# Kernel tuning notes

Hardware: AMD Instinct MI355X
Metric: run time of the kernel (lower is better)

Reference implementation:

```python
import jax, jax.numpy as jnp
import numpy as np

B, N, DIM = 32, 1024, 512
HEADS, HEAD_DIM = 8, 64
MLP_HIDDEN = 2048
MAX_DIST = 7
TABLE_SIZE = (2 * MAX_DIST + 1) ** 2  # 225


def setup_inputs() -> dict:
    key = jax.random.key(0)
    ks = jax.random.split(key, 8)
    return {
        "x": jax.random.normal(ks[0], (B, N, DIM), jnp.float32),
        "qkv_w": jax.random.normal(ks[1], (3 * DIM, DIM), jnp.float32) * 0.02,
        "proj_w": jax.random.normal(ks[2], (DIM, DIM), jnp.float32) * 0.02,
        "proj_b": jnp.zeros((DIM,), jnp.float32),
        "mlp_w1": jax.random.normal(ks[3], (MLP_HIDDEN, DIM), jnp.float32) * 0.02,
        "mlp_b1": jnp.zeros((MLP_HIDDEN,), jnp.float32),
        "mlp_w2": jax.random.normal(ks[4], (DIM, MLP_HIDDEN), jnp.float32) * 0.02,
        "mlp_b2": jnp.zeros((DIM,), jnp.float32),
        "norm1_g": jnp.ones((DIM,), jnp.float32),
        "norm1_b": jnp.zeros((DIM,), jnp.float32),
        "norm2_g": jnp.ones((DIM,), jnp.float32),
        "norm2_b": jnp.zeros((DIM,), jnp.float32),
        "bias_table": jax.random.normal(ks[5], (TABLE_SIZE, HEADS), jnp.float32) * 0.02,
        "height": 32,
        "width": 32,
    }


def _rel_pos_index(height, width):
    # exact replication of RelativePositionBias index math (numpy, trace-time)
    coords = np.stack(np.meshgrid(np.arange(height), np.arange(width), indexing="ij"))  # [2,H,W]
    flat = coords.reshape(2, -1)                         # [2,N]
    rel = flat[:, :, None] - flat[:, None, :]            # [2,N,N]
    rel = rel.transpose(1, 2, 0).copy()                  # [N,N,2]
    rel[:, :, 0] += height - 1
    rel[:, :, 1] += width - 1
    rel[:, :, 0] *= 2 * width - 1
    idx = np.clip(rel.sum(-1), 0, TABLE_SIZE - 1)
    return jnp.asarray(idx, jnp.int32)                   # [N,N]


def _layernorm(x, g, b, eps=1e-5):
    mu = x.mean(-1, keepdims=True)
    var = ((x - mu) ** 2).mean(-1, keepdims=True)
    return (x - mu) * jax.lax.rsqrt(var + eps) * g + b


def reference(x, qkv_w, proj_w, proj_b, mlp_w1, mlp_b1, mlp_w2, mlp_b2,
              norm1_g, norm1_b, norm2_g, norm2_b, bias_table, height, width):
    scale = HEAD_DIM ** -0.5
    idx = _rel_pos_index(height, width)
    bias = bias_table[idx]                               # [N,N,heads]
    bias = jnp.transpose(bias, (2, 0, 1))                # [heads,N,N]

    shortcut = x
    h = _layernorm(x, norm1_g, norm1_b)
    qkv = h @ qkv_w.T                                    # [B,N,3*DIM]
    qkv = qkv.reshape(x.shape[0], x.shape[1], 3, HEADS, HEAD_DIM)
    qkv = jnp.transpose(qkv, (2, 0, 3, 1, 4))            # [3,B,h,N,d]
    q, k, v = qkv[0], qkv[1], qkv[2]
    attn = jnp.einsum("bhnd,bhmd->bhnm", q, k) * scale
    attn = attn + bias[None]
    attn = jax.nn.softmax(attn, axis=-1)
    o = jnp.einsum("bhnm,bhmd->bhnd", attn, v)           # [B,h,N,d]
    o = jnp.transpose(o, (0, 2, 1, 3)).reshape(x.shape)  # [B,N,DIM]
    o = o @ proj_w.T + proj_b
    x = shortcut + o

    shortcut = x
    h = _layernorm(x, norm2_g, norm2_b)
    h = jax.nn.gelu(h @ mlp_w1.T + mlp_b1, approximate=False)
    h = h @ mlp_w2.T + mlp_b2
    return shortcut + h
```

## Files before the change

kernel.cpp:

```cpp
#include <hip/hip_runtime.h>

typedef short bf16x8 __attribute__((ext_vector_type(8)));
typedef float f32x4 __attribute__((ext_vector_type(4)));
typedef unsigned short us8 __attribute__((ext_vector_type(8)));
typedef unsigned short us2 __attribute__((ext_vector_type(2)));

__device__ __forceinline__ float bf2f(unsigned short u) {
    union { unsigned i; float f; } v; v.i = ((unsigned)u) << 16; return v.f;
}
__device__ __forceinline__ unsigned short f2bf(float f) {
    union { float f; unsigned i; } v; v.f = f;
    unsigned r = v.i + 0x7fffu + ((v.i >> 16) & 1u);
    return (unsigned short)(r >> 16);
}
__device__ __forceinline__ float ldflex(const void* p, int isf32, long i) {
    return isf32 ? ((const float*)p)[i] : bf2f(((const unsigned short*)p)[i]);
}
__device__ __forceinline__ float gelu_exact(float v) {
    return 0.5f * v * (1.0f + erff(v * 0.70710678118654752f));
}
__device__ __forceinline__ us8 pack8u(const float* s) {
    us8 r;
    #pragma unroll
    for (int i = 0; i < 8; ++i) r[i] = f2bf(s[i]);
    return r;
}

__device__ __forceinline__ void gld16(const void* g, void* l) {
    typedef __attribute__((address_space(1))) void GV;
    typedef __attribute__((address_space(3))) void LV;
    __builtin_amdgcn_global_load_lds((GV*)g, (LV*)l, 16, 0, 0);
}

struct SniffArgs { const void* p[13]; int n[13]; };

__global__ __launch_bounds__(64) void sniff_all(SniffArgs a, int* __restrict__ flags)
{
    const unsigned short* buf = (const unsigned short*)a.p[blockIdx.x];
    const int n_elems = a.n[blockIdx.x];
    __shared__ int cnt[3];
    if (threadIdx.x < 3) cnt[threadIdx.x] = 0;
    __syncthreads();
    int K = n_elems / 2; if (K > 1024) K = 1024; if (K < 1) K = 1;
    int ins = 0, ne = 0, no = 0;
    for (int i = threadIdx.x; i < K; i += 64) {
        const unsigned lo = buf[2 * i], hi = buf[2 * i + 1];
        const unsigned e = (lo >> 7) & 0xFF;
        ins += (lo != 0 && (e < 90 || e > 160)) ? 1 : 0;
        ne  += (lo != 0);
        no  += (hi != 0);
    }
    atomicAdd(&cnt[0], ins); atomicAdd(&cnt[1], ne); atomicAdd(&cnt[2], no);
    __syncthreads();
    if (threadIdx.x == 0)
        flags[blockIdx.x] = (cnt[0] * 10 > K) || (cnt[1] * 10 < K && cnt[2] * 2 > K);
}

struct CvtArgs { const void* src[7]; void* dst[7]; int fidx[7]; int n[7]; int tobf[7]; };

__global__ __launch_bounds__(256) void convert_params(CvtArgs a, const int* __restrict__ flags)
{
    const int t = blockIdx.y;
    const int i0 = (blockIdx.x * 256 + threadIdx.x) * 8;
    if (i0 >= a.n[t]) return;
    const int f = flags[a.fidx[t]];
    float v[8];
    if (f) {
        const float* s = (const float*)a.src[t] + i0;
        *(f32x4*)&v[0] = *(const f32x4*)s;
        *(f32x4*)&v[4] = *(const f32x4*)(s + 4);
    } else {
        us8 u = *(const us8*)((const unsigned short*)a.src[t] + i0);
        #pragma unroll
        for (int i = 0; i < 8; ++i) v[i] = bf2f(u[i]);
    }
    if (a.tobf[t]) {
        *(us8*)((unsigned short*)a.dst[t] + i0) = pack8u(v);
    } else {
        float* d = (float*)a.dst[t] + i0;
        *(f32x4*)d       = *(f32x4*)&v[0];
        *(f32x4*)(d + 4) = *(f32x4*)&v[4];
    }
}

__global__ __launch_bounds__(256) void gemm_bf16(
    const unsigned short* __restrict__ A, const unsigned short* __restrict__ W,
    void* __restrict__ C, int Nout, int K,
    const float* __restrict__ bias,
    const void* resid, const int* rflag, long resid_row0,
    int act, int out_bf16)
{
    __shared__ unsigned short As[128 * 32];
    __shared__ unsigned short Bs[128 * 32];
    const int tid  = threadIdx.x;
    const int lane = tid & 63, wv = tid >> 6;
    const int wrow = wv >> 1, wcol = wv & 1;
    const int fm = lane & 15, quad = lane >> 4;

    const int gx = gridDim.x;
    const int nwg = gx * gridDim.y;
    int lin = blockIdx.y * gx + blockIdx.x;
    lin = (lin & 7) * (nwg >> 3) + (lin >> 3);
    const int bm = (lin / gx) * 128, bn = (lin % gx) * 128;

    const int sr = tid >> 2;
    const int sb = (tid & 3) * 16;
    const char* Ab = (const char*)A;
    const char* Wb = (const char*)W;
    char* AsB = (char*)As;
    char* BsB = (char*)Bs;
    const long a0 = ((long)(bm + sr) * K) * 2 + sb;
    const long a1 = ((long)(bm + 64 + sr) * K) * 2 + sb;
    const long b0 = ((long)(bn + sr) * K) * 2 + sb;
    const long b1 = ((long)(bn + 64 + sr) * K) * 2 + sb;
    const int ld = tid * 16;

    f32x4 acc[4][4] = {};

    const int Kb = K * 2;
    for (int k0b = 0; k0b < Kb; k0b += 64) {
        __syncthreads();
        gld16(Ab + a0 + k0b, AsB + ld);
        gld16(Ab + a1 + k0b, AsB + 4096 + ld);
        gld16(Wb + b0 + k0b, BsB + ld);
        gld16(Wb + b1 + k0b, BsB + 4096 + ld);
        __syncthreads();

        bf16x8 af[4], bw[4];
        #pragma unroll
        for (int t = 0; t < 4; ++t) {
            af[t] = *(const bf16x8*)&As[(wrow * 64 + t * 16 + fm) * 32 + quad * 8];
            bw[t] = *(const bf16x8*)&Bs[(wcol * 64 + t * 16 + fm) * 32 + quad * 8];
        }
        #pragma unroll
        for (int i = 0; i < 4; ++i)
            #pragma unroll
            for (int j = 0; j < 4; ++j)
                acc[i][j] = __builtin_amdgcn_mfma_f32_16x16x32_bf16(
                                af[i], bw[j], acc[i][j], 0, 0, 0);
    }

    const int crow0 = bm + wrow * 64, ccol0 = bn + wcol * 64;
    if (out_bf16) {
        unsigned short* Cb = (unsigned short*)C;
        #pragma unroll
        for (int j = 0; j < 4; ++j) {
            const int col = ccol0 + j * 16 + fm;
            const float bv = bias ? bias[col] : 0.0f;
            #pragma unroll
            for (int i = 0; i < 4; ++i)
                #pragma unroll
                for (int r = 0; r < 4; ++r) {
                    const int row = crow0 + i * 16 + quad * 4 + r;
                    float v = acc[i][j][r] + bv;
                    if (act) v = gelu_exact(v);
                    Cb[(long)row * Nout + col] = f2bf(v);
                }
        }
    } else {
        float* Cf = (float*)C;
        const int rfl = resid ? (rflag ? *rflag : 1) : 1;
        #pragma unroll
        for (int j = 0; j < 4; ++j) {
            const int col = ccol0 + j * 16 + fm;
            const float bv = bias ? bias[col] : 0.0f;
            #pragma unroll
            for (int i = 0; i < 4; ++i)
                #pragma unroll
                for (int r = 0; r < 4; ++r) {
                    const int row = crow0 + i * 16 + quad * 4 + r;
                    float v = acc[i][j][r] + bv;
                    if (act)   v = gelu_exact(v);
                    if (resid) v += ldflex(resid, rfl, (resid_row0 + row) * (long)Nout + col);
                    Cf[(long)row * Nout + col] = v;
                }
        }
    }
}

__global__ __launch_bounds__(256) void layernorm_512(
    const void* __restrict__ x, const int* __restrict__ xflag, long row0,
    const void* __restrict__ g, const int* __restrict__ gflag,
    const void* __restrict__ b, const int* __restrict__ bflag,
    unsigned short* __restrict__ o)
{
    const int row = blockIdx.x;
    const int tid = threadIdx.x;
    const int xf = xflag ? *xflag : 1;
    const long base = (row0 + row) * 512 + tid * 2;
    const float vx = ldflex(x, xf, base);
    const float vy = ldflex(x, xf, base + 1);
    float s  = vx + vy;
    float s2 = vx * vx + vy * vy;
    #pragma unroll
    for (int off = 32; off > 0; off >>= 1) {
        s  += __shfl_down(s, off);
        s2 += __shfl_down(s2, off);
    }
    __shared__ float ss[4], ss2[4];
    if ((tid & 63) == 0) { ss[tid >> 6] = s; ss2[tid >> 6] = s2; }
    __syncthreads();
    const float ts   = ss[0] + ss[1] + ss[2] + ss[3];
    const float ts2  = ss2[0] + ss2[1] + ss2[2] + ss2[3];
    const float mean = ts * (1.0f / 512.0f);
    const float var  = ts2 * (1.0f / 512.0f) - mean * mean;
    const float rstd = rsqrtf(var + 1e-5f);
    const int gf = *gflag, bff = *bflag;
    us2 r;
    r[0] = f2bf((vx - mean) * rstd * ldflex(g, gf, tid * 2)     + ldflex(b, bff, tid * 2));
    r[1] = f2bf((vy - mean) * rstd * ldflex(g, gf, tid * 2 + 1) + ldflex(b, bff, tid * 2 + 1));
    *(us2*)(o + (long)row * 512 + tid * 2) = r;
}

__global__ __launch_bounds__(256, 5) void attn_mfma(
    const unsigned short* __restrict__ qkv,
    const void* __restrict__ table, const int* __restrict__ tflag,
    unsigned short* __restrict__ o)
{
    __shared__ unsigned short Ks[512 * 8];
    __shared__ unsigned short Vt[64 * 72];
    __shared__ unsigned short Pl[4][16 * 72];
    __shared__ float Tbh[225];

    const int tid  = threadIdx.x;
    const int lane = tid & 63, wv = tid >> 6;
    const int fm = lane & 15, quad = lane >> 4;

    const int hw    = blockIdx.x + gridDim.x * (blockIdx.y + gridDim.y * blockIdx.z);
    const int total = gridDim.x * gridDim.y * gridDim.z;
    const int lin   = (hw & 7) * (total >> 3) + (hw >> 3);
    const int q0 = (lin & 15) * 64;
    const int h  = (lin >> 4) & 7;
    const int b  = lin >> 7;

    {
        const int tf = *tflag;
        if (tid < 225) Tbh[tid] = ldflex(table, tf, tid * 8 + h);
    }

    bf16x8 qa[2];
    {
        const unsigned short* qb = &qkv[(long)((b * 1024 + q0 + wv * 16 + fm) * 3) * 512
                                        + h * 64 + quad * 8];
        qa[0] = *(const bf16x8*)qb;
        qa[1] = *(const bf16x8*)(qb + 32);
    }

    int base_r[4];
    #pragma unroll
    for (int r = 0; r < 4; ++r) {
        const int qi = q0 + wv * 16 + quad * 4 + r;
        base_r[r] = 63 * (qi >> 5) + (qi & 31) + 1984;
    }

    const int kc_fm   = tid & 15;
    const int kc_quad = (tid >> 4) & 3;
    const int kc_ch   = (tid >> 6) & 1;
    const int kc_c0   = (tid >> 7) & 1;
    const char* qkvB  = (const char*)qkv;
    long ksrc = (((long)(b * 1024 + kc_c0 * 16 + kc_fm) * 3 + 1) * 512
                 + h * 64 + kc_ch * 32 + kc_quad * 8) * 2;

    const int key_v = tid & 63;
    const int dv    = (tid >> 6) * 16;
    long vsrc = (((long)(b * 1024 + key_v) * 3 + 2) * 512 + h * 64 + dv) * 2;

    char* KsB = (char*)Ks;

    f32x4 acc[4] = {};
    float mrow[4] = {-1e30f, -1e30f, -1e30f, -1e30f};
    float lrow[4] = {};

    for (int kt = 0; kt < 16; ++kt) {
        const int k0 = kt * 64;
        __syncthreads();
        us8 v0 = *(const us8*)(qkvB + vsrc);
        us8 v1 = *(const us8*)(qkvB + vsrc + 16);
        gld16(qkvB + ksrc,         KsB + tid * 16);
        gld16(qkvB + ksrc + 98304, KsB + 4096 + tid * 16);
        ksrc += 196608; vsrc += 196608;
        #pragma unroll
        for (int i = 0; i < 8; ++i) Vt[(dv + i) * 72 + key_v] = v0[i];
        #pragma unroll
        for (int i = 0; i < 8; ++i) Vt[(dv + 8 + i) * 72 + key_v] = v1[i];
        __syncthreads();

        f32x4 sv[4];
        __builtin_amdgcn_s_setprio(1);
        #pragma unroll
        for (int c = 0; c < 4; ++c) {
            f32x4 z = {};
            z = __builtin_amdgcn_mfma_f32_16x16x32_bf16(
                    qa[0], *(const bf16x8*)&Ks[(((c * 2 + 0) * 4 + quad) * 16 + fm) * 8],
                    z, 0, 0, 0);
            z = __builtin_amdgcn_mfma_f32_16x16x32_bf16(
                    qa[1], *(const bf16x8*)&Ks[(((c * 2 + 1) * 4 + quad) * 16 + fm) * 8],
                    z, 0, 0, 0);
            sv[c] = z;
        }
        __builtin_amdgcn_s_setprio(0);

        #pragma unroll
        for (int c = 0; c < 4; ++c) {
            const int kj = k0 + c * 16 + fm;
            const int sub = 63 * (kj >> 5) + (kj & 31);
            #pragma unroll
            for (int r = 0; r < 4; ++r) {
                int idx = base_r[r] - sub;
                idx = idx > 224 ? 224 : idx;
                sv[c][r] = fmaf(sv[c][r], 0.125f, Tbh[idx]);
            }
        }

        float alpha[4];
        #pragma unroll
        for (int r = 0; r < 4; ++r) {
            float mr = fmaxf(fmaxf(sv[0][r], sv[1][r]), fmaxf(sv[2][r], sv[3][r]));
            #pragma unroll
            for (int off = 1; off < 16; off <<= 1) mr = fmaxf(mr, __shfl_xor(mr, off));
            const float mnew = fmaxf(mrow[r], mr);
            alpha[r] = __expf(mrow[r] - mnew);
            mrow[r] = mnew;
            float ps = 0.0f;
            #pragma unroll
            for (int c = 0; c < 4; ++c) {
                const float p = __expf(sv[c][r] - mnew);
                sv[c][r] = p;
                ps += p;
            }
            #pragma unroll
            for (int off = 1; off < 16; off <<= 1) ps += __shfl_xor(ps, off);
            lrow[r] = lrow[r] * alpha[r] + ps;
        }

        unsigned short* Pw = Pl[wv];
        #pragma unroll
        for (int c = 0; c < 4; ++c)
            #pragma unroll
            for (int r = 0; r < 4; ++r)
                Pw[(quad * 4 + r) * 72 + c * 16 + fm] = f2bf(sv[c][r]);

        const bf16x8 ap0 = *(const bf16x8*)&Pw[fm * 72 + quad * 8];
        const bf16x8 ap1 = *(const bf16x8*)&Pw[fm * 72 + 32 + quad * 8];
        __builtin_amdgcn_s_setprio(1);
        #pragma unroll
        for (int c = 0; c < 4; ++c) {
            #pragma unroll
            for (int r = 0; r < 4; ++r) acc[c][r] *= alpha[r];
            acc[c] = __builtin_amdgcn_mfma_f32_16x16x32_bf16(
                        ap0, *(const bf16x8*)&Vt[(c * 16 + fm) * 72 + quad * 8], acc[c], 0, 0, 0);
            acc[c] = __builtin_amdgcn_mfma_f32_16x16x32_bf16(
                        ap1, *(const bf16x8*)&Vt[(c * 16 + fm) * 72 + 32 + quad * 8], acc[c], 0, 0, 0);
        }
        __builtin_amdgcn_s_setprio(0);
    }

    float rinv[4];
    #pragma unroll
    for (int r = 0; r < 4; ++r) rinv[r] = 1.0f / lrow[r];
    #pragma unroll
    for (int c = 0; c < 4; ++c)
        #pragma unroll
        for (int r = 0; r < 4; ++r)
            o[(long)(b * 1024 + q0 + wv * 16 + quad * 4 + r) * 512 + h * 64 + c * 16 + fm]
                = f2bf(acc[c][r] * rinv[r]);
}

extern "C" void kernel_launch(void* const* d_in, const int* in_sizes, int n_in,
                              void* d_out, int out_size, void* d_ws, size_t ws_size,
                              hipStream_t stream)
{
    (void)n_in; (void)out_size;
    float* out = (float*)d_out;

    constexpr int B = 32, N = 1024;

    int* flags = (int*)d_ws;
    {
        SniffArgs sa;
        for (int t = 0; t < 13; ++t) { sa.p[t] = d_in[t]; sa.n[t] = in_sizes[t]; }
        sniff_all<<<13, 64, 0, stream>>>(sa, flags);
    }

    unsigned short* Wq = (unsigned short*)((char*)d_ws + 256);
    unsigned short* Wp = Wq + 786432;
    unsigned short* W1 = Wp + 262144;
    unsigned short* W2 = W1 + 1048576;
    float* Bp = (float*)(W2 + 1048576);
    float* B1 = Bp + 512;
    float* B2 = B1 + 2048;
    char* scr = (char*)(B2 + 512);
    scr = (char*)(((size_t)scr + 255) & ~(size_t)255);

    {
        CvtArgs ca;
        ca.src[0] = d_in[1]; ca.dst[0] = Wq; ca.fidx[0] = 1; ca.n[0] = 786432;  ca.tobf[0] = 1;
        ca.src[1] = d_in[2]; ca.dst[1] = Wp; ca.fidx[1] = 2; ca.n[1] = 262144;  ca.tobf[1] = 1;
        ca.src[2] = d_in[4]; ca.dst[2] = W1; ca.fidx[2] = 4; ca.n[2] = 1048576; ca.tobf[2] = 1;
        ca.src[3] = d_in[6]; ca.dst[3] = W2; ca.fidx[3] = 6; ca.n[3] = 1048576; ca.tobf[3] = 1;
        ca.src[4] = d_in[3]; ca.dst[4] = Bp; ca.fidx[4] = 3; ca.n[4] = 512;     ca.tobf[4] = 0;
        ca.src[5] = d_in[5]; ca.dst[5] = B1; ca.fidx[5] = 5; ca.n[5] = 2048;    ca.tobf[5] = 0;
        ca.src[6] = d_in[7]; ca.dst[6] = B2; ca.fidx[6] = 7; ca.n[6] = 512;     ca.tobf[6] = 0;
        convert_params<<<dim3(512, 7), 256, 0, stream>>>(ca, flags);
    }

    const size_t fixed = (size_t)(scr - (char*)d_ws);
    const size_t per_batch = (size_t)N * 3072 * 2;
    int bpc = (int)((ws_size - fixed) / per_batch);
    if (bpc < 1) bpc = 1;
    if (bpc > B) bpc = B;

    unsigned short* Ln = (unsigned short*)scr;
    unsigned short* Hd = Ln + (size_t)bpc * N * 512;
    unsigned short* Ao = Hd + (size_t)bpc * N * 2048;

    for (int b0 = 0; b0 < B; b0 += bpc) {
        const int nb   = (B - b0) < bpc ? (B - b0) : bpc;
        const int rows = nb * N;
        const long r0  = (long)b0 * N;

        layernorm_512<<<rows, 256, 0, stream>>>(
            d_in[0], flags + 0, r0, d_in[8], flags + 8, d_in[9], flags + 9, Ln);
        gemm_bf16<<<dim3(12, rows / 128), 256, 0, stream>>>(
            Ln, Wq, Hd, 1536, 512, nullptr, nullptr, nullptr, 0, 0, 1);
        attn_mfma<<<dim3(16, 8, nb), 256, 0, stream>>>(
            Hd, d_in[12], flags + 12, Ao);
        gemm_bf16<<<dim3(4, rows / 128), 256, 0, stream>>>(
            Ao, Wp, out + r0 * 512, 512, 512,
            Bp, d_in[0], flags + 0, r0, 0, 0);
    }

    for (int b0 = 0; b0 < B; b0 += bpc) {
        const int nb   = (B - b0) < bpc ? (B - b0) : bpc;
        const int rows = nb * N;
        const long r0  = (long)b0 * N;

        layernorm_512<<<rows, 256, 0, stream>>>(
            out + r0 * 512, nullptr, 0, d_in[10], flags + 10, d_in[11], flags + 11, Ln);
        gemm_bf16<<<dim3(16, rows / 128), 256, 0, stream>>>(
            Ln, W1, Hd, 2048, 512, B1, nullptr, nullptr, 0, 1, 1);
        gemm_bf16<<<dim3(4, rows / 128), 256, 0, stream>>>(
            Hd, W2, out + r0 * 512, 512, 2048,
            B2, out + r0 * 512, nullptr, 0, 0, 0);
    }
}
```

Before: 938.9 us.

## Double-buffer GEMM LDS tiles and restructure attention loads, bias, rowsum and packing

The GEMM now double-buffers its A/W LDS tiles, issuing the next k-slice load before the MFMAs and keeping one barrier per iteration. The attention kernel register-prefetches the next K/V tile, reads the relative-position bias from incrementally updated indices with contiguous table reads, and computes the softmax row sum with an MFMA against a ones vector instead of shuffle reductions. It also converts to bf16 with v_cvt_pk_bf16_f32 for the P tile and the output. The costs are more LDS (lower GEMM occupancy), more registers for prefetch, and the bf16-rounded P being used in the row sum.

```diff
diff --git a/kernel.cpp b/kernel.cpp
--- a/kernel.cpp
+++ b/kernel.cpp
@@ -24,6 +24,11 @@
     #pragma unroll
     for (int i = 0; i < 8; ++i) r[i] = f2bf(s[i]);
     return r;
+}
+__device__ __forceinline__ unsigned cvtpk_bf16(float lo, float hi) {
+    unsigned u;
+    asm("v_cvt_pk_bf16_f32 %0, %1, %2" : "=v"(u) : "v"(lo), "v"(hi));
+    return u;
 }
 
 __device__ __forceinline__ void gld16(const void* g, void* l) {
@@ -90,8 +95,8 @@
     const void* resid, const int* rflag, long resid_row0,
     int act, int out_bf16)
 {
-    __shared__ unsigned short As[128 * 32];
-    __shared__ unsigned short Bs[128 * 32];
+    __shared__ unsigned short As[2][128 * 32];
+    __shared__ unsigned short Bs[2][128 * 32];
     const int tid  = threadIdx.x;
     const int lane = tid & 63, wv = tid >> 6;
     const int wrow = wv >> 1, wcol = wv & 1;
@@ -107,30 +112,37 @@
     const int sb = (tid & 3) * 16;
     const char* Ab = (const char*)A;
     const char* Wb = (const char*)W;
-    char* AsB = (char*)As;
-    char* BsB = (char*)Bs;
     const long a0 = ((long)(bm + sr) * K) * 2 + sb;
     const long a1 = ((long)(bm + 64 + sr) * K) * 2 + sb;
     const long b0 = ((long)(bn + sr) * K) * 2 + sb;
     const long b1 = ((long)(bn + 64 + sr) * K) * 2 + sb;
     const int ld = tid * 16;
 
+    auto stage = [&](int bsel, int k0b) {
+        char* AD = (char*)As[bsel];
+        char* BD = (char*)Bs[bsel];
+        gld16(Ab + a0 + k0b, AD + ld);
+        gld16(Ab + a1 + k0b, AD + 4096 + ld);
+        gld16(Wb + b0 + k0b, BD + ld);
+        gld16(Wb + b1 + k0b, BD + 4096 + ld);
+    };
+
     f32x4 acc[4][4] = {};
-
     const int Kb = K * 2;
+
+    stage(0, 0);
+    __syncthreads();
+    int cur = 0;
     for (int k0b = 0; k0b < Kb; k0b += 64) {
-        __syncthreads();
-        gld16(Ab + a0 + k0b, AsB + ld);
-        gld16(Ab + a1 + k0b, AsB + 4096 + ld);
-        gld16(Wb + b0 + k0b, BsB + ld);
-        gld16(Wb + b1 + k0b, BsB + 4096 + ld);
-        __syncthreads();
-
+        if (k0b + 64 < Kb) stage(cur ^ 1, k0b + 64);
+
+        const unsigned short* Ac = As[cur];
+        const unsigned short* Bc = Bs[cur];
         bf16x8 af[4], bw[4];
         #pragma unroll
         for (int t = 0; t < 4; ++t) {
-            af[t] = *(const bf16x8*)&As[(wrow * 64 + t * 16 + fm) * 32 + quad * 8];
-            bw[t] = *(const bf16x8*)&Bs[(wcol * 64 + t * 16 + fm) * 32 + quad * 8];
+            af[t] = *(const bf16x8*)&Ac[(wrow * 64 + t * 16 + fm) * 32 + quad * 8];
+            bw[t] = *(const bf16x8*)&Bc[(wcol * 64 + t * 16 + fm) * 32 + quad * 8];
         }
         #pragma unroll
         for (int i = 0; i < 4; ++i)
@@ -138,6 +150,8 @@
             for (int j = 0; j < 4; ++j)
                 acc[i][j] = __builtin_amdgcn_mfma_f32_16x16x32_bf16(
                                 af[i], bw[j], acc[i][j], 0, 0, 0);
+        __syncthreads();
+        cur ^= 1;
     }
 
     const int crow0 = bm + wrow * 64, ccol0 = bn + wcol * 64;
@@ -220,7 +234,7 @@
     __shared__ unsigned short Ks[512 * 8];
     __shared__ unsigned short Vt[64 * 72];
     __shared__ unsigned short Pl[4][16 * 72];
-    __shared__ float Tbh[225];
+    __shared__ float Tbh[228];
 
     const int tid  = threadIdx.x;
     const int lane = tid & 63, wv = tid >> 6;
@@ -235,7 +249,10 @@
 
     {
         const int tf = *tflag;
-        if (tid < 225) Tbh[tid] = ldflex(table, tf, tid * 8 + h);
+        if (tid < 228) {
+            const int src = tid > 224 ? 224 : tid;
+            Tbh[tid] = ldflex(table, tf, src * 8 + h);
+        }
     }
 
     bf16x8 qa[2];
@@ -246,12 +263,18 @@
         qa[1] = *(const bf16x8*)(qb + 32);
     }
 
-    int base_r[4];
-    #pragma unroll
-    for (int r = 0; r < 4; ++r) {
-        const int qi = q0 + wv * 16 + quad * 4 + r;
-        base_r[r] = 63 * (qi >> 5) + (qi & 31) + 1984;
-    }
+    const int qi0   = q0 + wv * 16 + quad * 4;
+    const int base0 = 63 * (qi0 >> 5) + (qi0 & 31) + 1984;
+    int idxr[4];
+    #pragma unroll
+    for (int c = 0; c < 4; ++c) {
+        const int kj = c * 16 + fm;
+        idxr[c] = base0 - (63 * (kj >> 5) + (kj & 31));
+    }
+
+    bf16x8 ones8;
+    #pragma unroll
+    for (int i = 0; i < 8; ++i) ones8[i] = (short)0x3F80;
 
     const int kc_fm   = tid & 15;
     const int kc_quad = (tid >> 4) & 3;
@@ -268,22 +291,34 @@
     char* KsB = (char*)Ks;
 
     f32x4 acc[4] = {};
+    f32x4 accS = {};
     float mrow[4] = {-1e30f, -1e30f, -1e30f, -1e30f};
-    float lrow[4] = {};
+
+    us8 kv0 = *(const us8*)(qkvB + ksrc);
+    us8 kv1 = *(const us8*)(qkvB + ksrc + 98304);
+    us8 vv0 = *(const us8*)(qkvB + vsrc);
+    us8 vv1 = *(const us8*)(qkvB + vsrc + 16);
 
     for (int kt = 0; kt < 16; ++kt) {
-        const int k0 = kt * 64;
         __syncthreads();
-        us8 v0 = *(const us8*)(qkvB + vsrc);
-        us8 v1 = *(const us8*)(qkvB + vsrc + 16);
-        gld16(qkvB + ksrc,         KsB + tid * 16);
-        gld16(qkvB + ksrc + 98304, KsB + 4096 + tid * 16);
-        ksrc += 196608; vsrc += 196608;
-        #pragma unroll
-        for (int i = 0; i < 8; ++i) Vt[(dv + i) * 72 + key_v] = v0[i];
-        #pragma unroll
-        for (int i = 0; i < 8; ++i) Vt[(dv + 8 + i) * 72 + key_v] = v1[i];
-        __syncthreads();
+
+        *(us8*)(KsB + tid * 16)        = kv0;
+        *(us8*)(KsB + 4096 + tid * 16) = kv1;
+        #pragma unroll
+        for (int i = 0; i < 8; ++i) Vt[(dv + i) * 72 + key_v]     = vv0[i];
+        #pragma unroll
+        for (int i = 0; i < 8; ++i) Vt[(dv + 8 + i) * 72 + key_v] = vv1[i];
+
+        if (kt < 15) {
+            ksrc += 196608; vsrc += 196608;
+            kv0 = *(const us8*)(qkvB + ksrc);
+            kv1 = *(const us8*)(qkvB + ksrc + 98304);
+            vv0 = *(const us8*)(qkvB + vsrc);
+            vv1 = *(const us8*)(qkvB + vsrc + 16);
+        }
+
+        asm volatile("s_waitcnt lgkmcnt(0)" ::: "memory");
+        __builtin_amdgcn_s_barrier();
 
         f32x4 sv[4];
         __builtin_amdgcn_s_setprio(1);
@@ -302,14 +337,12 @@
 
         #pragma unroll
         for (int c = 0; c < 4; ++c) {
-            const int kj = k0 + c * 16 + fm;
-            const int sub = 63 * (kj >> 5) + (kj & 31);
-            #pragma unroll
-            for (int r = 0; r < 4; ++r) {
-                int idx = base_r[r] - sub;
-                idx = idx > 224 ? 224 : idx;
-                sv[c][r] = fmaf(sv[c][r], 0.125f, Tbh[idx]);
-            }
+            const int i0 = idxr[c] > 224 ? 224 : idxr[c];
+            const float* tb = &Tbh[i0];
+            idxr[c] -= 126;
+            #pragma unroll
+            for (int r = 0; r < 4; ++r)
+                sv[c][r] = fmaf(sv[c][r], 0.125f, tb[r]);
         }
 
         float alpha[4];
@@ -321,24 +354,22 @@
             const float mnew = fmaxf(mrow[r], mr);
             alpha[r] = __expf(mrow[r] - mnew);
             mrow[r] = mnew;
-            float ps = 0.0f;
-            #pragma unroll
-            for (int c = 0; c < 4; ++c) {
-                const float p = __expf(sv[c][r] - mnew);
-                sv[c][r] = p;
-                ps += p;
-            }
-            #pragma unroll
-            for (int off = 1; off < 16; off <<= 1) ps += __shfl_xor(ps, off);
-            lrow[r] = lrow[r] * alpha[r] + ps;
+            #pragma unroll
+            for (int c = 0; c < 4; ++c)
+                sv[c][r] = __expf(sv[c][r] - mnew);
         }
 
         unsigned short* Pw = Pl[wv];
         #pragma unroll
-        for (int c = 0; c < 4; ++c)
-            #pragma unroll
-            for (int r = 0; r < 4; ++r)
-                Pw[(quad * 4 + r) * 72 + c * 16 + fm] = f2bf(sv[c][r]);
+        for (int r = 0; r < 4; ++r) {
+            const unsigned u01 = cvtpk_bf16(sv[0][r], sv[1][r]);
+            const unsigned u23 = cvtpk_bf16(sv[2][r], sv[3][r]);
+            const int row = (quad * 4 + r) * 72;
+            Pw[row + fm]      = (unsigned short)u01;
+            Pw[row + 16 + fm] = (unsigned short)(u01 >> 16);
+            Pw[row + 32 + fm] = (unsigned short)u23;
+            Pw[row + 48 + fm] = (unsigned short)(u23 >> 16);
+        }
 
         const bf16x8 ap0 = *(const bf16x8*)&Pw[fm * 72 + quad * 8];
         const bf16x8 ap1 = *(const bf16x8*)&Pw[fm * 72 + 32 + quad * 8];
@@ -352,18 +383,26 @@
             acc[c] = __builtin_amdgcn_mfma_f32_16x16x32_bf16(
                         ap1, *(const bf16x8*)&Vt[(c * 16 + fm) * 72 + 32 + quad * 8], acc[c], 0, 0, 0);
         }
+        #pragma unroll
+        for (int r = 0; r < 4; ++r) accS[r] *= alpha[r];
+        accS = __builtin_amdgcn_mfma_f32_16x16x32_bf16(ap0, ones8, accS, 0, 0, 0);
+        accS = __builtin_amdgcn_mfma_f32_16x16x32_bf16(ap1, ones8, accS, 0, 0, 0);
         __builtin_amdgcn_s_setprio(0);
     }
 
     float rinv[4];
     #pragma unroll
-    for (int r = 0; r < 4; ++r) rinv[r] = 1.0f / lrow[r];
-    #pragma unroll
-    for (int c = 0; c < 4; ++c)
-        #pragma unroll
-        for (int r = 0; r < 4; ++r)
-            o[(long)(b * 1024 + q0 + wv * 16 + quad * 4 + r) * 512 + h * 64 + c * 16 + fm]
-                = f2bf(acc[c][r] * rinv[r]);
+    for (int r = 0; r < 4; ++r) rinv[r] = 1.0f / accS[r];
+    #pragma unroll
+    for (int r = 0; r < 4; ++r) {
+        const long ob = (long)(b * 1024 + q0 + wv * 16 + quad * 4 + r) * 512 + h * 64;
+        const unsigned u01 = cvtpk_bf16(acc[0][r] * rinv[r], acc[1][r] * rinv[r]);
+        const unsigned u23 = cvtpk_bf16(acc[2][r] * rinv[r], acc[3][r] * rinv[r]);
+        o[ob + fm]      = (unsigned short)u01;
+        o[ob + 16 + fm] = (unsigned short)(u01 >> 16);
+        o[ob + 32 + fm] = (unsigned short)u23;
+        o[ob + 48 + fm] = (unsigned short)(u23 >> 16);
+    }
 }
 
 extern "C" void kernel_launch(void* const* d_in, const int* in_sizes, int n_in,
```

New measurement: 858.0 us. 1.09x faster.
